# Kernel optimization log

Hardware: AMD Instinct MI355X
Metric: run time of the kernel (lower is better)

The kernel has to match this reference:

```python
import jax, jax.numpy as jnp
import numpy as np

# Dimensions: B=batch, T=decode len, S=source len, E=emb, H=rnn hidden, ENC=encoder size, V=vocab
B, T, S, E, H, ENC, V = 32, 64, 128, 256, 512, 512, 32000


def setup_inputs() -> dict:
    key = jax.random.key(0)
    ks = jax.random.split(key, 12)
    sc = lambda k, shape, s: jax.random.normal(k, shape, jnp.float32) * s
    return {
        "gold_tokens": jax.random.randint(ks[0], (B, T), 0, V),
        "enc_outputs": jax.random.normal(ks[1], (B, S, ENC), jnp.float32),
        "enc_lengths": jax.random.randint(ks[2], (B,), S // 2, S + 1),
        "h0": jnp.zeros((B, H), jnp.float32),
        "c0": jnp.zeros((B, H), jnp.float32),
        # learned parameters
        "embed_table": sc(ks[3], (V, E), 0.02),
        "W_ih": sc(ks[4], (4 * H, E), 0.05),   # torch LSTM gate order: i, f, g, o
        "W_hh": sc(ks[5], (4 * H, H), 0.05),
        "b_ih": jnp.zeros((4 * H,), jnp.float32),
        "b_hh": jnp.zeros((4 * H,), jnp.float32),
        "Wa": sc(ks[6], (H, ENC), 0.05),        # 'general' attention: score = q^T Wa k
        "Wc_w": sc(ks[7], (H, H + ENC), 0.05),  # Wc: Linear(rnn+enc -> ho=rnn)
        "Wc_b": jnp.zeros((H,), jnp.float32),
        "Wo_w": sc(ks[8], (V, H), 0.02),        # Wo: Linear(ho -> vocab)
        "Wo_b": jnp.zeros((V,), jnp.float32),
    }


def reference(gold_tokens, enc_outputs, enc_lengths, h0, c0, embed_table,
              W_ih, W_hh, b_ih, b_hh, Wa, Wc_w, Wc_b, Wo_w, Wo_b):
    S = enc_outputs.shape[1]
    # length mask for attention over encoder states
    mask = jnp.arange(S)[None, :] < enc_lengths[:, None]          # [B, S]
    # precompute Wa @ enc (invariant across decode steps)
    proj_enc = jnp.einsum('he,bse->bsh', Wa, enc_outputs)         # [B, S, H]
    embs = embed_table[gold_tokens]                               # [B, T, E] teacher forcing

    def step(carry, e_t):
        h, c = carry                                              # [B, H] each
        gates = e_t @ W_ih.T + b_ih + h @ W_hh.T + b_hh           # [B, 4H]
        i, f, g, o = jnp.split(gates, 4, axis=-1)
        c = jax.nn.sigmoid(f) * c + jax.nn.sigmoid(i) * jnp.tanh(g)
        h = jax.nn.sigmoid(o) * jnp.tanh(c)
        # general attention: score[b,s] = h[b] . (Wa enc[b,s])
        scores = jnp.einsum('bh,bsh->bs', h, proj_enc)
        scores = jnp.where(mask, scores, jnp.float32(-1e9))
        att = jax.nn.softmax(scores, axis=-1)                     # [B, S]
        ctx = jnp.einsum('bs,bse->be', att, enc_outputs)          # [B, ENC]
        ho = jnp.concatenate([h, ctx], axis=-1) @ Wc_w.T + Wc_b   # [B, H]
        logit = ho @ Wo_w.T + Wo_b                                # [B, V]
        return (h, c), logit

    (_, _), logits = jax.lax.scan(step, (h0, c0), jnp.swapaxes(embs, 0, 1))
    return jnp.swapaxes(logits, 0, 1)                             # [B, T, V]
```

## Files before the change

### kernel.cpp

```cpp
#include <hip/hip_runtime.h>

typedef unsigned short u16;
typedef unsigned int   u32;
typedef unsigned long long u64;
typedef __attribute__((ext_vector_type(8))) __bf16 bf16x8;
typedef __attribute__((ext_vector_type(4))) float  f32x4;

#define B_   32
#define T_   64
#define S_   128
#define E_   256
#define H_   512
#define ENC_ 512
#define V_   32000

__device__ __forceinline__ float b2f(u16 u) {
  union { u32 i; float f; } v; v.i = ((u32)u) << 16; return v.f;
}
__device__ __forceinline__ u16 f2b(float f) {
  union { float f; u32 i; } v; v.f = f;
  u32 r = (v.i + 0x7fffu + ((v.i >> 16) & 1u)) >> 16;
  return (u16)r;
}
__device__ __forceinline__ float sigm(float x) { return 1.f / (1.f + __expf(-x)); }

__device__ __forceinline__ void async_ld16(const void* g, void* l) {
  __builtin_amdgcn_global_load_lds((const __attribute__((address_space(1))) u32*)g,
                                   (__attribute__((address_space(3))) u32*)l,
                                   16, 0, 0);
}

__global__ __launch_bounds__(256) void k_cvt(const float* __restrict__ src,
                                             u16* __restrict__ dst, int n4) {
  int i = blockIdx.x * 256 + threadIdx.x;
  if (i < n4) {
    float4 v = ((const float4*)src)[i];
    ushort4 o;
    o.x = f2b(v.x); o.y = f2b(v.y); o.z = f2b(v.z); o.w = f2b(v.w);
    ((ushort4*)dst)[i] = o;
  }
}

template <typename OUT_T>
__global__ __launch_bounds__(256) void gemm_bt(
    const u16* __restrict__ A, int lda,
    const u16* __restrict__ B, int ldb,
    OUT_T* __restrict__ C, int ldc, int K,
    const float* __restrict__ bias1, const float* __restrict__ bias2) {
  __shared__ __align__(16) u16 As[128 * 64];
  __shared__ __align__(16) u16 Bs[128 * 64];

  const int tid  = threadIdx.x;
  int f = blockIdx.y * gridDim.x + blockIdx.x;
  const int nwg = gridDim.x * gridDim.y;
  int g = (nwg & 7) ? f : ((f & 7) * (nwg >> 3) + (f >> 3));
  const int m0 = (g % gridDim.x) * 128;
  const int n0 = (g / gridDim.x) * 128;
  const int wave = tid >> 6, lane = tid & 63;
  const int mw = (wave >> 1) * 64, nw = (wave & 1) * 64;
  const int lr = lane & 15, lq = lane >> 4;

  f32x4 acc[4][4];
#pragma unroll
  for (int i = 0; i < 4; ++i)
#pragma unroll
    for (int j = 0; j < 4; ++j) acc[i][j] = (f32x4){0.f, 0.f, 0.f, 0.f};

  for (int k0 = 0; k0 < K; k0 += 64) {
#pragma unroll
    for (int it = 0; it < 4; ++it) {
      int chunk = it * 256 + tid;
      int row = chunk >> 3;
      int kc  = (chunk & 7) << 3;
      async_ld16(&A[(size_t)(m0 + row) * lda + k0 + kc], &As[chunk << 3]);
    }
#pragma unroll
    for (int it = 0; it < 4; ++it) {
      int chunk = it * 256 + tid;
      int row = chunk >> 3;
      int kc  = (chunk & 7) << 3;
      async_ld16(&B[(size_t)(n0 + row) * ldb + k0 + kc], &Bs[chunk << 3]);
    }
    __syncthreads();
#pragma unroll
    for (int kk = 0; kk < 2; ++kk) {
      bf16x8 af[4], bf[4];
#pragma unroll
      for (int i = 0; i < 4; ++i)
        af[i] = *(const bf16x8*)&As[(mw + i * 16 + lr) * 64 + kk * 32 + lq * 8];
#pragma unroll
      for (int j = 0; j < 4; ++j)
        bf[j] = *(const bf16x8*)&Bs[(nw + j * 16 + lr) * 64 + kk * 32 + lq * 8];
#pragma unroll
      for (int i = 0; i < 4; ++i)
#pragma unroll
        for (int j = 0; j < 4; ++j)
          acc[i][j] = __builtin_amdgcn_mfma_f32_16x16x32_bf16(af[i], bf[j], acc[i][j], 0, 0, 0);
    }
    __syncthreads();
  }

#pragma unroll
  for (int j = 0; j < 4; ++j) {
    int n = n0 + nw + j * 16 + lr;
    float bs = 0.f;
    if (bias1) bs += bias1[n];
    if (bias2) bs += bias2[n];
#pragma unroll
    for (int i = 0; i < 4; ++i) {
#pragma unroll
      for (int r = 0; r < 4; ++r) {
        int m = m0 + mw + i * 16 + lq * 4 + r;
        float v = acc[i][j][r] + bs;
        if constexpr (sizeof(OUT_T) == 2)
          C[(size_t)m * ldc + n] = (OUT_T)f2b(v);
        else
          C[(size_t)m * ldc + n] = v;
      }
    }
  }
}

template <typename OUT_T>
__global__ __launch_bounds__(256) void gemm64(
    const u16* __restrict__ A, int lda,
    const u16* __restrict__ B, int ldb,
    OUT_T* __restrict__ C, int ldc, int K,
    const float* __restrict__ bias1, const float* __restrict__ bias2) {
  __shared__ __align__(16) u16 As[64 * 64];
  __shared__ __align__(16) u16 Bs[64 * 64];

  const int tid  = threadIdx.x;
  int f = blockIdx.y * gridDim.x + blockIdx.x;
  const int nwg = gridDim.x * gridDim.y;
  int g = (nwg & 7) ? f : ((f & 7) * (nwg >> 3) + (f >> 3));
  const int m0 = (g % gridDim.x) * 64;
  const int n0 = (g / gridDim.x) * 64;
  const int wave = tid >> 6, lane = tid & 63;
  const int mw = (wave >> 1) * 32, nw = (wave & 1) * 32;
  const int lr = lane & 15, lq = lane >> 4;

  f32x4 acc[2][2];
#pragma unroll
  for (int i = 0; i < 2; ++i)
#pragma unroll
    for (int j = 0; j < 2; ++j) acc[i][j] = (f32x4){0.f, 0.f, 0.f, 0.f};

  for (int k0 = 0; k0 < K; k0 += 64) {
#pragma unroll
    for (int it = 0; it < 2; ++it) {
      int chunk = it * 256 + tid;
      int row = chunk >> 3;
      int kc  = (chunk & 7) << 3;
      async_ld16(&A[(size_t)(m0 + row) * lda + k0 + kc], &As[chunk << 3]);
    }
#pragma unroll
    for (int it = 0; it < 2; ++it) {
      int chunk = it * 256 + tid;
      int row = chunk >> 3;
      int kc  = (chunk & 7) << 3;
      async_ld16(&B[(size_t)(n0 + row) * ldb + k0 + kc], &Bs[chunk << 3]);
    }
    __syncthreads();
#pragma unroll
    for (int kk = 0; kk < 2; ++kk) {
      bf16x8 af[2], bf[2];
#pragma unroll
      for (int i = 0; i < 2; ++i)
        af[i] = *(const bf16x8*)&As[(mw + i * 16 + lr) * 64 + kk * 32 + lq * 8];
#pragma unroll
      for (int j = 0; j < 2; ++j)
        bf[j] = *(const bf16x8*)&Bs[(nw + j * 16 + lr) * 64 + kk * 32 + lq * 8];
#pragma unroll
      for (int i = 0; i < 2; ++i)
#pragma unroll
        for (int j = 0; j < 2; ++j)
          acc[i][j] = __builtin_amdgcn_mfma_f32_16x16x32_bf16(af[i], bf[j], acc[i][j], 0, 0, 0);
    }
    __syncthreads();
  }

#pragma unroll
  for (int j = 0; j < 2; ++j) {
    int n = n0 + nw + j * 16 + lr;
    float bs = 0.f;
    if (bias1) bs += bias1[n];
    if (bias2) bs += bias2[n];
#pragma unroll
    for (int i = 0; i < 2; ++i) {
#pragma unroll
      for (int r = 0; r < 4; ++r) {
        int m = m0 + mw + i * 16 + lq * 4 + r;
        float v = acc[i][j][r] + bs;
        if constexpr (sizeof(OUT_T) == 2)
          C[(size_t)m * ldc + n] = (OUT_T)f2b(v);
        else
          C[(size_t)m * ldc + n] = v;
      }
    }
  }
}

__global__ __launch_bounds__(256) void k_embed(const int* __restrict__ toks,
                                               const float* __restrict__ table,
                                               u16* __restrict__ emb) {
  int id  = blockIdx.x * 256 + threadIdx.x;
  int row = id >> 6;
  int c4  = (id & 63) << 2;
  int tok = toks[row];
  float4 v = *(const float4*)&table[(size_t)tok * E_ + c4];
  ushort4 o;
  o.x = f2b(v.x); o.y = f2b(v.y); o.z = f2b(v.z); o.w = f2b(v.w);
  *(ushort4*)&emb[(size_t)row * E_ + c4] = o;
}

__global__ __launch_bounds__(256) void k_transpose(const float* __restrict__ Wa,
                                                   u16* __restrict__ WaT) {
  __shared__ float tle[32][33];
  int bx = blockIdx.x * 32;
  int by = blockIdx.y * 32;
  int tid = threadIdx.x;
  for (int i = tid; i < 1024; i += 256) {
    int r = i >> 5, c = i & 31;
    tle[r][c] = Wa[(size_t)(bx + r) * ENC_ + by + c];
  }
  __syncthreads();
  for (int i = tid; i < 1024; i += 256) {
    int r = i >> 5, c = i & 31;
    WaT[(size_t)(by + r) * H_ + bx + c] = f2b(tle[c][r]);
  }
}

__global__ __launch_bounds__(256) void k_lstm(
    const u16* __restrict__ Whh,
    const float* __restrict__ gp,
    const float* __restrict__ c0,
    u16* __restrict__ Hbuf,
    u16* __restrict__ hc) {
  const int blk  = blockIdx.x;
  const int tid  = threadIdx.x;
  const int wave = tid >> 6, lane = tid & 63;
  const int mi = wave >> 1, ni = wave & 1;
  const int lr = lane & 15, lq = lane >> 4;

  const int p    = ni * 16 + lr;
  const int grow = (p >> 3) * H_ + blk * 8 + (p & 7);
  bf16x8 bfr[16];
#pragma unroll
  for (int ks = 0; ks < 16; ++ks)
    bfr[ks] = *(const bf16x8*)&Whh[(size_t)grow * H_ + ks * 32 + lq * 8];

  const int pb = tid >> 3, pj = tid & 7;
  const int hidx = blk * 8 + pj;
  float c = c0[pb * H_ + hidx];

  __shared__ float G[32][33];

  const int am = mi * 16 + lr;

  u64 af8[32];
  {
    const u64* a0p = (const u64*)((const char*)Hbuf + (size_t)am * 1024 + lq * 16);
#pragma unroll
    for (int ks = 0; ks < 16; ++ks) {
      af8[2 * ks]     = a0p[ks * 8];
      af8[2 * ks + 1] = a0p[ks * 8 + 1];
    }
  }

  float gpr[4];
#pragma unroll
  for (int r = 0; r < 4; ++r)
    gpr[r] = gp[(size_t)((mi * 16 + lq * 4 + r) * T_ + 0) * 2048 + grow];

  for (int t = 0; t < T_; ++t) {
    f32x4 acc = (f32x4){0.f, 0.f, 0.f, 0.f};
#pragma unroll
    for (int ks = 0; ks < 16; ++ks) {
      union { u64 q[2]; bf16x8 v; } uu;
      uu.q[0] = af8[2 * ks]; uu.q[1] = af8[2 * ks + 1];
      acc = __builtin_amdgcn_mfma_f32_16x16x32_bf16(uu.v, bfr[ks], acc, 0, 0, 0);
    }
    __syncthreads();
#pragma unroll
    for (int r = 0; r < 4; ++r)
      G[mi * 16 + lq * 4 + r][p] = acc[r] + gpr[r];
    __syncthreads();

    if (t < T_ - 1) {
#pragma unroll
      for (int r = 0; r < 4; ++r)
        gpr[r] = gp[(size_t)((mi * 16 + lq * 4 + r) * T_ + t + 1) * 2048 + grow];
    }

    float gi = G[pb][pj], gf = G[pb][8 + pj], gg = G[pb][16 + pj], go = G[pb][24 + pj];
    c = sigm(gf) * c + sigm(gi) * tanhf(gg);
    float h = sigm(go) * tanhf(c);
    u16 hb = f2b(h);
    u32 other = (u32)__shfl_xor((int)(u32)hb, 1);
    if (!(tid & 1)) {
      u32 pk = (u32)hb | (other << 16);
      __hip_atomic_store((u32*)&Hbuf[(size_t)(t + 1) * (B_ * H_) + pb * H_ + hidx], pk,
                         __ATOMIC_RELAXED, __HIP_MEMORY_SCOPE_AGENT);
      *(u32*)&hc[(size_t)(pb * T_ + t) * 1024 + hidx] = pk;
    }

    if (t < T_ - 1) {
      __builtin_amdgcn_s_sleep(12);
      const u64* hsrc = (const u64*)((const char*)Hbuf +
          ((size_t)(t + 1) * (B_ * H_) + (size_t)am * H_) * 2 + lq * 16);
#pragma unroll
      for (int ks = 0; ks < 16; ++ks) {
        af8[2 * ks] = __hip_atomic_load(&hsrc[ks * 8], __ATOMIC_RELAXED,
                                        __HIP_MEMORY_SCOPE_AGENT);
        af8[2 * ks + 1] = __hip_atomic_load(&hsrc[ks * 8 + 1], __ATOMIC_RELAXED,
                                            __HIP_MEMORY_SCOPE_AGENT);
      }
      for (;;) {
        u32 bad = 0;
#pragma unroll
        for (int i = 0; i < 32; ++i) bad |= (af8[i] == ~0ull);
        if (!bad) break;
        __builtin_amdgcn_s_sleep(2);
#pragma unroll
        for (int i = 0; i < 32; ++i)
          if (af8[i] == ~0ull)
            af8[i] = __hip_atomic_load(&hsrc[(i >> 1) * 8 + (i & 1)],
                                       __ATOMIC_RELAXED, __HIP_MEMORY_SCOPE_AGENT);
      }
    }
  }
}

__global__ __launch_bounds__(256) void k_attn(
    const u16* __restrict__ q,
    const u16* __restrict__ enc,
    const int* __restrict__ lens,
    u16* __restrict__ hc) {
  const int bt = blockIdx.x;
  const int b  = bt >> 6;
  const int tid = threadIdx.x;
  const int len = lens[b];

  __shared__ float qs[512];
  __shared__ float sc[128];
  __shared__ float red2[256];
  __shared__ float sred[2];

  for (int i = tid; i < 512; i += 256) qs[i] = b2f(q[(size_t)bt * 512 + i]);
  __syncthreads();

  {
    int s = tid & 127, half = tid >> 7;
    const u16* er = &enc[((size_t)b * S_ + s) * 512 + half * 256];
    const float* qb = &qs[half * 256];
    float a = 0.f;
#pragma unroll 4
    for (int k = 0; k < 256; k += 8) {
      uint4 raw = *(const uint4*)&er[k];
      u32 w0 = raw.x, w1 = raw.y, w2 = raw.z, w3 = raw.w;
      union { u32 i; float f; } lo, hi;
      lo.i = w0 << 16;          a += lo.f * qb[k + 0];
      hi.i = w0 & 0xffff0000u;  a += hi.f * qb[k + 1];
      lo.i = w1 << 16;          a += lo.f * qb[k + 2];
      hi.i = w1 & 0xffff0000u;  a += hi.f * qb[k + 3];
      lo.i = w2 << 16;          a += lo.f * qb[k + 4];
      hi.i = w2 & 0xffff0000u;  a += hi.f * qb[k + 5];
      lo.i = w3 << 16;          a += lo.f * qb[k + 6];
      hi.i = w3 & 0xffff0000u;  a += hi.f * qb[k + 7];
    }
    red2[tid] = a;
  }
  __syncthreads();
  if (tid < 128) {
    float v = red2[tid] + red2[tid + 128];
    sc[tid] = (tid < len) ? v : -1e30f;
  }
  __syncthreads();
  if (tid < 64) {
    float m = fmaxf(sc[tid], sc[tid + 64]);
#pragma unroll
    for (int o = 32; o > 0; o >>= 1) m = fmaxf(m, __shfl_down(m, o));
    if (tid == 0) sred[0] = m;
  }
  __syncthreads();
  float mx = sred[0];
  if (tid < 128) sc[tid] = __expf(sc[tid] - mx);
  __syncthreads();
  if (tid < 64) {
    float s2 = sc[tid] + sc[tid + 64];
#pragma unroll
    for (int o = 32; o > 0; o >>= 1) s2 += __shfl_down(s2, o);
    if (tid == 0) sred[1] = s2;
  }
  __syncthreads();
  float inv = 1.0f / sred[1];

  float a0 = 0.f, a1 = 0.f;
  for (int s = 0; s < S_; ++s) {
    float at = sc[s];
    const u16* er = &enc[((size_t)b * S_ + s) * 512];
    a0 += at * b2f(er[tid]);
    a1 += at * b2f(er[tid + 256]);
  }
  hc[(size_t)bt * 1024 + 512 + tid]       = f2b(a0 * inv);
  hc[(size_t)bt * 1024 + 512 + tid + 256] = f2b(a1 * inv);
}

extern "C" void kernel_launch(void* const* d_in, const int* in_sizes, int n_in,
                              void* d_out, int out_size, void* d_ws, size_t ws_size,
                              hipStream_t stream) {
  const int*   toks  = (const int*)d_in[0];
  const float* enc   = (const float*)d_in[1];
  const int*   lens  = (const int*)d_in[2];
  const float* h0    = (const float*)d_in[3];
  const float* c0    = (const float*)d_in[4];
  const float* table = (const float*)d_in[5];
  const float* W_ih  = (const float*)d_in[6];
  const float* W_hh  = (const float*)d_in[7];
  const float* b_ih  = (const float*)d_in[8];
  const float* b_hh  = (const float*)d_in[9];
  const float* Wa    = (const float*)d_in[10];
  const float* Wc_w  = (const float*)d_in[11];
  const float* Wc_b  = (const float*)d_in[12];
  const float* Wo_w  = (const float*)d_in[13];
  const float* Wo_b  = (const float*)d_in[14];
  float* out = (float*)d_out;

  char* ws = (char*)d_ws;
  size_t off = 0;
  auto alloc = [&](size_t bytes) {
    void* pp = ws + off;
    off += (bytes + 255) & ~(size_t)255;
    return pp;
  };
  float* gp    = (float*)alloc((size_t)B_ * T_ * 2048 * 4);
  u16*   emb   = (u16*)alloc((size_t)B_ * T_ * E_ * 2);
  u16*   Hbuf  = (u16*)alloc((size_t)(T_ + 1) * B_ * H_ * 2);
  u16*   hc    = (u16*)alloc((size_t)B_ * T_ * 1024 * 2);
  u16*   q     = (u16*)alloc((size_t)B_ * T_ * ENC_ * 2);
  u16*   WaT   = (u16*)alloc((size_t)ENC_ * H_ * 2);
  u16*   ho    = (u16*)alloc((size_t)B_ * T_ * H_ * 2);
  u16*   Wihb  = (u16*)alloc((size_t)2048 * E_ * 2);
  u16*   Whhb  = (u16*)alloc((size_t)2048 * H_ * 2);
  u16*   Wcwb  = (u16*)alloc((size_t)H_ * 1024 * 2);
  u16*   Wowb  = (u16*)alloc((size_t)V_ * H_ * 2);
  u16*   encb  = (u16*)alloc((size_t)B_ * S_ * ENC_ * 2);
  (void)in_sizes; (void)n_in; (void)out_size; (void)ws_size;

  hipMemsetAsync(Hbuf + (size_t)B_ * H_, 0xFF, (size_t)T_ * B_ * H_ * 2, stream);

  k_cvt<<<(2048 * E_ / 4 + 255) / 256, 256, 0, stream>>>(W_ih, Wihb, 2048 * E_ / 4);
  k_cvt<<<(2048 * H_ / 4 + 255) / 256, 256, 0, stream>>>(W_hh, Whhb, 2048 * H_ / 4);
  k_cvt<<<(H_ * 1024 / 4 + 255) / 256, 256, 0, stream>>>(Wc_w, Wcwb, H_ * 1024 / 4);
  k_cvt<<<(V_ * H_ / 4 + 255) / 256, 256, 0, stream>>>(Wo_w, Wowb, V_ * H_ / 4);
  k_cvt<<<(B_ * S_ * ENC_ / 4 + 255) / 256, 256, 0, stream>>>(enc, encb, B_ * S_ * ENC_ / 4);
  k_cvt<<<(B_ * H_ / 4 + 255) / 256, 256, 0, stream>>>(h0, Hbuf, B_ * H_ / 4);
  k_embed<<<512, 256, 0, stream>>>(toks, table, emb);
  gemm_bt<float><<<dim3(16, 16), 256, 0, stream>>>(emb, E_, Wihb, E_, gp, 2048, E_, b_ih, b_hh);
  k_transpose<<<dim3(16, 16), 256, 0, stream>>>(Wa, WaT);
  k_lstm<<<64, 256, 0, stream>>>(Whhb, gp, c0, Hbuf, hc);
  gemm64<u16><<<dim3(32, 8), 256, 0, stream>>>(hc, 1024, WaT, H_, q, ENC_, H_, nullptr, nullptr);
  k_attn<<<B_ * T_, 256, 0, stream>>>(q, encb, lens, hc);
  gemm64<u16><<<dim3(32, 8), 256, 0, stream>>>(hc, 1024, Wcwb, 1024, ho, H_, 1024, Wc_b, nullptr);
  gemm_bt<float><<<dim3(16, 250), 256, 0, stream>>>(ho, H_, Wowb, H_, out, V_, H_, Wo_b, nullptr);
}
```

Baseline: 944.4 us.

## Stage LSTM hidden state in LDS, merge conversion kernels, vectorize attention context

The LSTM recurrence changes how it fetches the new hidden state. Before, each lane spun on scattered per-lane atomic loads into registers after a fixed sleep. Now all threads cooperatively load the whole hidden-state slab with coalesced polling and stage it in LDS, so MFMA operands are read from shared memory. This adds an extra barrier per step and LDS traffic. Separately, six bf16 conversion launches become a single multi-job kernel, and the attention context loop reads packed bf16 pairs with 32-bit loads.

```diff
diff --git a/kernel.cpp b/kernel.cpp
--- a/kernel.cpp
+++ b/kernel.cpp
@@ -30,15 +30,26 @@
                                    16, 0, 0);
 }
 
-__global__ __launch_bounds__(256) void k_cvt(const float* __restrict__ src,
-                                             u16* __restrict__ dst, int n4) {
+struct CvtJobs {
+  const float* src[6];
+  u16*         dst[6];
+  int          end[6];
+};
+
+__global__ __launch_bounds__(256) void k_cvt_all(CvtJobs j) {
   int i = blockIdx.x * 256 + threadIdx.x;
-  if (i < n4) {
-    float4 v = ((const float4*)src)[i];
-    ushort4 o;
-    o.x = f2b(v.x); o.y = f2b(v.y); o.z = f2b(v.z); o.w = f2b(v.w);
-    ((ushort4*)dst)[i] = o;
-  }
+  if (i >= j.end[5]) return;
+  const float* s; u16* d; int local;
+  if      (i < j.end[0]) { s = j.src[0]; d = j.dst[0]; local = i; }
+  else if (i < j.end[1]) { s = j.src[1]; d = j.dst[1]; local = i - j.end[0]; }
+  else if (i < j.end[2]) { s = j.src[2]; d = j.dst[2]; local = i - j.end[1]; }
+  else if (i < j.end[3]) { s = j.src[3]; d = j.dst[3]; local = i - j.end[2]; }
+  else if (i < j.end[4]) { s = j.src[4]; d = j.dst[4]; local = i - j.end[3]; }
+  else                   { s = j.src[5]; d = j.dst[5]; local = i - j.end[4]; }
+  float4 v = ((const float4*)s)[local];
+  ushort4 o;
+  o.x = f2b(v.x); o.y = f2b(v.y); o.z = f2b(v.z); o.w = f2b(v.w);
+  ((ushort4*)d)[local] = o;
 }
 
 template <typename OUT_T>
@@ -254,45 +265,34 @@
   const int hidx = blk * 8 + pj;
   float c = c0[pb * H_ + hidx];
 
+  __shared__ __align__(16) u16 Hs[32 * 512];
   __shared__ float G[32][33];
 
   const int am = mi * 16 + lr;
-
-  u64 af8[32];
-  {
-    const u64* a0p = (const u64*)((const char*)Hbuf + (size_t)am * 1024 + lq * 16);
-#pragma unroll
-    for (int ks = 0; ks < 16; ++ks) {
-      af8[2 * ks]     = a0p[ks * 8];
-      af8[2 * ks + 1] = a0p[ks * 8 + 1];
-    }
-  }
 
   float gpr[4];
 #pragma unroll
   for (int r = 0; r < 4; ++r)
     gpr[r] = gp[(size_t)((mi * 16 + lq * 4 + r) * T_ + 0) * 2048 + grow];
 
+#pragma unroll
+  for (int it = 0; it < 8; ++it) {
+    int chunk = it * 256 + tid;
+    async_ld16(&Hbuf[chunk * 8], &Hs[chunk * 8]);
+  }
+  __syncthreads();
+
   for (int t = 0; t < T_; ++t) {
     f32x4 acc = (f32x4){0.f, 0.f, 0.f, 0.f};
 #pragma unroll
     for (int ks = 0; ks < 16; ++ks) {
-      union { u64 q[2]; bf16x8 v; } uu;
-      uu.q[0] = af8[2 * ks]; uu.q[1] = af8[2 * ks + 1];
-      acc = __builtin_amdgcn_mfma_f32_16x16x32_bf16(uu.v, bfr[ks], acc, 0, 0, 0);
-    }
-    __syncthreads();
+      bf16x8 a = *(const bf16x8*)&Hs[am * H_ + ks * 32 + lq * 8];
+      acc = __builtin_amdgcn_mfma_f32_16x16x32_bf16(a, bfr[ks], acc, 0, 0, 0);
+    }
 #pragma unroll
     for (int r = 0; r < 4; ++r)
       G[mi * 16 + lq * 4 + r][p] = acc[r] + gpr[r];
     __syncthreads();
-
-    if (t < T_ - 1) {
-#pragma unroll
-      for (int r = 0; r < 4; ++r)
-        gpr[r] = gp[(size_t)((mi * 16 + lq * 4 + r) * T_ + t + 1) * 2048 + grow];
-    }
-
     float gi = G[pb][pj], gf = G[pb][8 + pj], gg = G[pb][16 + pj], go = G[pb][24 + pj];
     c = sigm(gf) * c + sigm(gi) * tanhf(gg);
     float h = sigm(go) * tanhf(c);
@@ -306,28 +306,36 @@
     }
 
     if (t < T_ - 1) {
-      __builtin_amdgcn_s_sleep(12);
-      const u64* hsrc = (const u64*)((const char*)Hbuf +
-          ((size_t)(t + 1) * (B_ * H_) + (size_t)am * H_) * 2 + lq * 16);
-#pragma unroll
-      for (int ks = 0; ks < 16; ++ks) {
-        af8[2 * ks] = __hip_atomic_load(&hsrc[ks * 8], __ATOMIC_RELAXED,
-                                        __HIP_MEMORY_SCOPE_AGENT);
-        af8[2 * ks + 1] = __hip_atomic_load(&hsrc[ks * 8 + 1], __ATOMIC_RELAXED,
-                                            __HIP_MEMORY_SCOPE_AGENT);
-      }
+#pragma unroll
+      for (int r = 0; r < 4; ++r)
+        gpr[r] = gp[(size_t)((mi * 16 + lq * 4 + r) * T_ + t + 1) * 2048 + grow];
+      const u64* h8 = (const u64*)&Hbuf[(size_t)(t + 1) * (B_ * H_)];
+      u64 tmp[16];
+#pragma unroll
+      for (int it = 0; it < 16; ++it)
+        tmp[it] = __hip_atomic_load(&h8[it * 256 + tid], __ATOMIC_RELAXED,
+                                    __HIP_MEMORY_SCOPE_AGENT);
       for (;;) {
         u32 bad = 0;
 #pragma unroll
-        for (int i = 0; i < 32; ++i) bad |= (af8[i] == ~0ull);
+        for (int it = 0; it < 16; ++it) {
+          u32 lo = (u32)tmp[it], hi = (u32)(tmp[it] >> 32);
+          bad |= (lo == 0xFFFFFFFFu) | (hi == 0xFFFFFFFFu);
+        }
         if (!bad) break;
-        __builtin_amdgcn_s_sleep(2);
-#pragma unroll
-        for (int i = 0; i < 32; ++i)
-          if (af8[i] == ~0ull)
-            af8[i] = __hip_atomic_load(&hsrc[(i >> 1) * 8 + (i & 1)],
-                                       __ATOMIC_RELAXED, __HIP_MEMORY_SCOPE_AGENT);
+        __builtin_amdgcn_s_sleep(1);
+#pragma unroll
+        for (int it = 0; it < 16; ++it) {
+          u32 lo = (u32)tmp[it], hi = (u32)(tmp[it] >> 32);
+          if (lo == 0xFFFFFFFFu || hi == 0xFFFFFFFFu)
+            tmp[it] = __hip_atomic_load(&h8[it * 256 + tid], __ATOMIC_RELAXED,
+                                        __HIP_MEMORY_SCOPE_AGENT);
+        }
       }
+#pragma unroll
+      for (int it = 0; it < 16; ++it)
+        *(u64*)&Hs[(size_t)(it * 256 + tid) * 4] = tmp[it];
+      __syncthreads();
     }
   }
 }
@@ -397,14 +405,18 @@
   float inv = 1.0f / sred[1];
 
   float a0 = 0.f, a1 = 0.f;
+  const u16* eb = &enc[(size_t)b * S_ * 512 + 2 * tid];
+#pragma unroll 4
   for (int s = 0; s < S_; ++s) {
     float at = sc[s];
-    const u16* er = &enc[((size_t)b * S_ + s) * 512];
-    a0 += at * b2f(er[tid]);
-    a1 += at * b2f(er[tid + 256]);
-  }
-  hc[(size_t)bt * 1024 + 512 + tid]       = f2b(a0 * inv);
-  hc[(size_t)bt * 1024 + 512 + tid + 256] = f2b(a1 * inv);
+    u32 w = *(const u32*)&eb[(size_t)s * 512];
+    union { u32 i; float f; } lo, hi;
+    lo.i = w << 16; hi.i = w & 0xffff0000u;
+    a0 += at * lo.f;
+    a1 += at * hi.f;
+  }
+  u32 pk = (u32)f2b(a0 * inv) | ((u32)f2b(a1 * inv) << 16);
+  *(u32*)&hc[(size_t)bt * 1024 + 512 + 2 * tid] = pk;
 }
 
 extern "C" void kernel_launch(void* const* d_in, const int* in_sizes, int n_in,
@@ -450,12 +462,20 @@
 
   hipMemsetAsync(Hbuf + (size_t)B_ * H_, 0xFF, (size_t)T_ * B_ * H_ * 2, stream);
 
-  k_cvt<<<(2048 * E_ / 4 + 255) / 256, 256, 0, stream>>>(W_ih, Wihb, 2048 * E_ / 4);
-  k_cvt<<<(2048 * H_ / 4 + 255) / 256, 256, 0, stream>>>(W_hh, Whhb, 2048 * H_ / 4);
-  k_cvt<<<(H_ * 1024 / 4 + 255) / 256, 256, 0, stream>>>(Wc_w, Wcwb, H_ * 1024 / 4);
-  k_cvt<<<(V_ * H_ / 4 + 255) / 256, 256, 0, stream>>>(Wo_w, Wowb, V_ * H_ / 4);
-  k_cvt<<<(B_ * S_ * ENC_ / 4 + 255) / 256, 256, 0, stream>>>(enc, encb, B_ * S_ * ENC_ / 4);
-  k_cvt<<<(B_ * H_ / 4 + 255) / 256, 256, 0, stream>>>(h0, Hbuf, B_ * H_ / 4);
+  CvtJobs j;
+  int e0 = 2048 * E_ / 4;
+  int e1 = e0 + 2048 * H_ / 4;
+  int e2 = e1 + H_ * 1024 / 4;
+  int e3 = e2 + V_ * H_ / 4;
+  int e4 = e3 + B_ * S_ * ENC_ / 4;
+  int e5 = e4 + B_ * H_ / 4;
+  j.src[0] = W_ih; j.dst[0] = Wihb; j.end[0] = e0;
+  j.src[1] = W_hh; j.dst[1] = Whhb; j.end[1] = e1;
+  j.src[2] = Wc_w; j.dst[2] = Wcwb; j.end[2] = e2;
+  j.src[3] = Wo_w; j.dst[3] = Wowb; j.end[3] = e3;
+  j.src[4] = enc;  j.dst[4] = encb; j.end[4] = e4;
+  j.src[5] = h0;   j.dst[5] = Hbuf; j.end[5] = e5;
+  k_cvt_all<<<(e5 + 255) / 256, 256, 0, stream>>>(j);
   k_embed<<<512, 256, 0, stream>>>(toks, table, emb);
   gemm_bt<float><<<dim3(16, 16), 256, 0, stream>>>(emb, E_, Wihb, E_, gp, 2048, E_, b_ih, b_hh);
   k_transpose<<<dim3(16, 16), 256, 0, stream>>>(Wa, WaT);
```

Measured after the change: 828.1 us. -12.3%, faster.
